# Performance work log

Measured on AMD Instinct MI355X. Metric: run time of the kernel, lower is better.

## Reference

```python
import jax, jax.numpy as jnp
import numpy as np

N = 20000
E = 320000
NODE_DIM = 9
EDGE_DIM = 4
HID = 64
EHID = 32  # hidden_dim // 2, edge feature dim inside GAT layers
HEADS = 4
OUT_DIM = 256
NUM_LAYERS = 3


def layer_norm(x, g, b, eps=1e-5):
    m = jnp.mean(x, axis=-1, keepdims=True)
    v = jnp.mean((x - m) ** 2, axis=-1, keepdims=True)
    return (x - m) / jnp.sqrt(v + eps) * g + b


def setup_inputs():
    key = jax.random.key(0)
    ks = iter(jax.random.split(key, 48))
    def w(shape, scale=0.1):
        return jax.random.normal(next(ks), shape, dtype=jnp.float32) * scale
    inp = {
        "x": jax.random.normal(next(ks), (N, NODE_DIM), dtype=jnp.float32),
        "edge_attr": jax.random.normal(next(ks), (E, EDGE_DIM), dtype=jnp.float32),
        "edge_index": jax.random.randint(next(ks), (2, E), 0, N, dtype=jnp.int32),
        # node encoder: Linear(9,32)+ReLU+Linear(32,64)+LayerNorm(64)
        "ne_w1": w((NODE_DIM, 32)), "ne_b1": jnp.zeros((32,), jnp.float32),
        "ne_w2": w((32, HID)), "ne_b2": jnp.zeros((HID,), jnp.float32),
        "ne_g": jnp.ones((HID,), jnp.float32), "ne_beta": jnp.zeros((HID,), jnp.float32),
        # edge encoder: Linear(4,16)+ReLU+Linear(16,32)+LayerNorm(32)
        "ee_w1": w((EDGE_DIM, 16)), "ee_b1": jnp.zeros((16,), jnp.float32),
        "ee_w2": w((16, EHID)), "ee_b2": jnp.zeros((EHID,), jnp.float32),
        "ee_g": jnp.ones((EHID,), jnp.float32), "ee_beta": jnp.zeros((EHID,), jnp.float32),
        # risk attention: Linear(96,64)+Tanh+Linear(64,1)+Sigmoid
        "ra_w1": w((HID + EHID, HID)), "ra_b1": jnp.zeros((HID,), jnp.float32),
        "ra_w2": w((HID, 1)), "ra_b2": jnp.zeros((1,), jnp.float32),
        # GAT layers (stacked over NUM_LAYERS; identical shapes)
        "gat_wl": w((NUM_LAYERS, HID, HEADS * HID)),       # linear (no bias)
        "gat_wa": w((NUM_LAYERS, 2 * HID + EHID)),          # attention (out=1, no bias)
        "gat_we": w((NUM_LAYERS, EHID, HEADS * HID)),       # edge_transform (no bias)
        "gat_wo": w((NUM_LAYERS, HID, HID)),                # output_transform weight
        "gat_wob": jnp.zeros((NUM_LAYERS, HID), jnp.float32),
        # output layer: Linear(64,128)+ReLU+Linear(128,256)+LayerNorm(256)
        "ow_1": w((HID, 128)), "ob_1": jnp.zeros((128,), jnp.float32),
        "ow_2": w((128, OUT_DIM)), "ob_2": jnp.zeros((OUT_DIM,), jnp.float32),
        "o_g": jnp.ones((OUT_DIM,), jnp.float32), "o_beta": jnp.zeros((OUT_DIM,), jnp.float32),
    }
    return inp


def reference(x, edge_attr, edge_index,
              ne_w1, ne_b1, ne_w2, ne_b2, ne_g, ne_beta,
              ee_w1, ee_b1, ee_w2, ee_b2, ee_g, ee_beta,
              ra_w1, ra_b1, ra_w2, ra_b2,
              gat_wl, gat_wa, gat_we, gat_wo, gat_wob,
              ow_1, ob_1, ow_2, ob_2, o_g, o_beta):
    row, col = edge_index[0], edge_index[1]
    # encoders
    h = layer_norm(jax.nn.relu(x @ ne_w1 + ne_b1) @ ne_w2 + ne_b2, ne_g, ne_beta)            # [N, 64]
    ef = layer_norm(jax.nn.relu(edge_attr @ ee_w1 + ee_b1) @ ee_w2 + ee_b2, ee_g, ee_beta)   # [E, 32]
    # risk weights per edge
    ri = jnp.concatenate([h[row], ef], axis=1)                                                # [E, 96]
    rw = jax.nn.sigmoid(jnp.tanh(ri @ ra_w1 + ra_b1) @ ra_w2 + ra_b2)                         # [E, 1]
    xh = h
    for l in range(NUM_LAYERS):
        xproj = (xh @ gat_wl[l]).reshape(N, HEADS, HID)                                       # [N, H, 64]
        emsg = (ef @ gat_we[l]).reshape(E, HEADS, HID)                                        # [E, H, 64]
        # attention Linear(2*64+32 -> 1) split into three slices; avoids materializing the
        # [E, H, 160] concat. Same math: cat([x_i, x_j, ef]) @ wa.
        wa_i = gat_wa[l][:HID]
        wa_j = gat_wa[l][HID:2 * HID]
        wa_e = gat_wa[l][2 * HID:]
        x_j = xproj[col]                                                                      # [E, H, 64]
        alpha = xproj[row] @ wa_i + x_j @ wa_j + (ef @ wa_e)[:, None]                         # [E, H]
        alpha = jnp.where(alpha >= 0, alpha, 0.2 * alpha)  # leaky_relu(0.2)
        alpha = alpha * rw                                  # risk modulation (broadcast [E,1])
        alpha = jax.nn.softmax(alpha, axis=0)               # softmax over ALL edges per head (as in torch code)
        agg = jax.ops.segment_sum(alpha[:, :, None] * (x_j + emsg), col, num_segments=N)      # [N, H, 64]
        xh = jax.nn.relu(agg.mean(axis=1) @ gat_wo[l] + gat_wob[l])                           # [N, 64]
    out = layer_norm(jax.nn.relu(xh @ ow_1 + ob_1) @ ow_2 + ob_2, o_g, o_beta)                # [N, 256]
    return out
```

## Files before the change

kernel.cpp:

```cpp
#include <hip/hip_runtime.h>
#include <math.h>

#define NN 20000
#define EE 320000
#define HID 64
#define EHID 32
#define HEADS 4

__device__ __forceinline__ float fast_tanh(float x) {
  float e = __expf(2.f * x);
  return 1.f - 2.f * __builtin_amdgcn_rcpf(e + 1.f);
}
__device__ __forceinline__ float fast_sigmoid(float x) {
  return __builtin_amdgcn_rcpf(1.f + __expf(-x));
}
__device__ __forceinline__ float bcast8(float v, int q) {
  switch (q) {
    case 0: return __int_as_float(__builtin_amdgcn_ds_swizzle(__float_as_int(v), (0 << 5) | 0x18));
    case 1: return __int_as_float(__builtin_amdgcn_ds_swizzle(__float_as_int(v), (1 << 5) | 0x18));
    case 2: return __int_as_float(__builtin_amdgcn_ds_swizzle(__float_as_int(v), (2 << 5) | 0x18));
    case 3: return __int_as_float(__builtin_amdgcn_ds_swizzle(__float_as_int(v), (3 << 5) | 0x18));
    case 4: return __int_as_float(__builtin_amdgcn_ds_swizzle(__float_as_int(v), (4 << 5) | 0x18));
    case 5: return __int_as_float(__builtin_amdgcn_ds_swizzle(__float_as_int(v), (5 << 5) | 0x18));
    case 6: return __int_as_float(__builtin_amdgcn_ds_swizzle(__float_as_int(v), (6 << 5) | 0x18));
    default: return __int_as_float(__builtin_amdgcn_ds_swizzle(__float_as_int(v), (7 << 5) | 0x18));
  }
}

__global__ __launch_bounds__(256) void k_node_enc(
    const float* __restrict__ x, const float* __restrict__ w1, const float* __restrict__ b1,
    const float* __restrict__ w2, const float* __restrict__ b2,
    const float* __restrict__ g, const float* __restrict__ beta,
    float* __restrict__ h) {
  int n = blockIdx.x * blockDim.x + threadIdx.x;
  if (n >= NN) return;
  float xin[9];
#pragma unroll
  for (int k = 0; k < 9; k++) xin[k] = x[n * 9 + k];
  float hid[32];
#pragma unroll
  for (int j = 0; j < 32; j++) {
    float a = b1[j];
#pragma unroll
    for (int k = 0; k < 9; k++) a += xin[k] * w1[k * 32 + j];
    hid[j] = fmaxf(a, 0.f);
  }
  float o[64];
  float s = 0.f;
  for (int j = 0; j < 64; j++) {
    float a = b2[j];
#pragma unroll
    for (int k = 0; k < 32; k++) a += hid[k] * w2[k * 64 + j];
    o[j] = a;
    s += a;
  }
  float m = s * (1.f / 64.f);
  float v = 0.f;
  for (int j = 0; j < 64; j++) { float d = o[j] - m; v += d * d; }
  v *= (1.f / 64.f);
  float inv = rsqrtf(v + 1e-5f);
#pragma unroll
  for (int j4 = 0; j4 < 16; j4++) {
    float4 r;
    r.x = (o[j4 * 4 + 0] - m) * inv * g[j4 * 4 + 0] + beta[j4 * 4 + 0];
    r.y = (o[j4 * 4 + 1] - m) * inv * g[j4 * 4 + 1] + beta[j4 * 4 + 1];
    r.z = (o[j4 * 4 + 2] - m) * inv * g[j4 * 4 + 2] + beta[j4 * 4 + 2];
    r.w = (o[j4 * 4 + 3] - m) * inv * g[j4 * 4 + 3] + beta[j4 * 4 + 3];
    ((float4*)&h[n * 64])[j4] = r;
  }
}

__global__ __launch_bounds__(256) void k_hist(const int* __restrict__ ei, int* __restrict__ counts) {
  int e = blockIdx.x * 256 + threadIdx.x;
  if (e < EE) atomicAdd(&counts[ei[EE + e]], 1);
}
__global__ __launch_bounds__(1024) void k_scan(
    const int* __restrict__ counts, int* __restrict__ rowptr, int* __restrict__ cursor) {
  __shared__ int wsum[16];
  int t = threadIdx.x, lane = t & 63, w = t >> 6;
  const int CH = 20;
  int base_i = t * CH;
  int local = 0;
  for (int i = 0; i < CH; i++) {
    int idx = base_i + i;
    if (idx < NN) local += counts[idx];
  }
  int v = local;
#pragma unroll
  for (int off = 1; off < 64; off <<= 1) {
    int u = __shfl_up(v, off);
    if (lane >= off) v += u;
  }
  if (lane == 63) wsum[w] = v;
  __syncthreads();
  int wbase = 0;
  for (int i = 0; i < w; i++) wbase += wsum[i];
  int run = wbase + v - local;
  for (int i = 0; i < CH; i++) {
    int idx = base_i + i;
    if (idx < NN) {
      rowptr[idx] = run;
      cursor[idx] = run;
      run += counts[idx];
    }
  }
  if (t == 1023) rowptr[NN] = EE;
}

__global__ __launch_bounds__(256) void k_edge_enc(
    const float* __restrict__ ea, const float* __restrict__ w1, const float* __restrict__ b1,
    const float* __restrict__ w2, const float* __restrict__ b2,
    const float* __restrict__ g, const float* __restrict__ beta,
    const float* __restrict__ gat_wa, const int* __restrict__ ei,
    int* __restrict__ cursor,
    float* __restrict__ efs, float4* __restrict__ devs4, int2* __restrict__ rcs) {
  int e = blockIdx.x * blockDim.x + threadIdx.x;
  if (e >= EE) return;
  int row = ei[e], col = ei[EE + e];
  int pos = atomicAdd(&cursor[col], 1);
  float4 xin = ((const float4*)ea)[e];
  float hid[16];
#pragma unroll
  for (int j = 0; j < 16; j++) {
    float a = b1[j];
    a += xin.x * w1[0 * 16 + j];
    a += xin.y * w1[1 * 16 + j];
    a += xin.z * w1[2 * 16 + j];
    a += xin.w * w1[3 * 16 + j];
    hid[j] = fmaxf(a, 0.f);
  }
  float o[32];
  float s = 0.f;
#pragma unroll
  for (int j = 0; j < 32; j++) {
    float a = b2[j];
#pragma unroll
    for (int k = 0; k < 16; k++) a += hid[k] * w2[k * 32 + j];
    o[j] = a;
    s += a;
  }
  float m = s * (1.f / 32.f);
  float v = 0.f;
#pragma unroll
  for (int j = 0; j < 32; j++) { float d = o[j] - m; v += d * d; }
  v *= (1.f / 32.f);
  float inv = rsqrtf(v + 1e-5f);
  float d0 = 0.f, d1 = 0.f, d2 = 0.f;
  float vn[32];
#pragma unroll
  for (int j = 0; j < 32; j++) {
    vn[j] = (o[j] - m) * inv * g[j] + beta[j];
    d0 += vn[j] * gat_wa[0 * 160 + 128 + j];
    d1 += vn[j] * gat_wa[1 * 160 + 128 + j];
    d2 += vn[j] * gat_wa[2 * 160 + 128 + j];
  }
#pragma unroll
  for (int j4 = 0; j4 < 8; j4++) {
    float4 r;
    r.x = vn[j4 * 4 + 0]; r.y = vn[j4 * 4 + 1]; r.z = vn[j4 * 4 + 2]; r.w = vn[j4 * 4 + 3];
    ((float4*)&efs[(size_t)pos * 32])[j4] = r;
  }
  devs4[pos] = make_float4(d0, d1, d2, 0.f);
  rcs[pos] = make_int2(row, col);
}

__global__ __launch_bounds__(256) void k_risk_node(
    const float* __restrict__ h, const float* __restrict__ w1, const float* __restrict__ b1,
    float* __restrict__ hnode) {
  __shared__ float xsT[64][20];
  int t = threadIdx.x;
  int n0 = blockIdx.x * 16;
  const float4* h4 = (const float4*)h;
  {
    int m = t & 15, k4 = t >> 4;
    float4 xv = h4[(n0 + m) * 16 + k4];
    xsT[k4 * 4 + 0][m] = xv.x;
    xsT[k4 * 4 + 1][m] = xv.y;
    xsT[k4 * 4 + 2][m] = xv.z;
    xsT[k4 * 4 + 3][m] = xv.w;
  }
  __syncthreads();
  int j = t & 63, grp = t >> 6;
  float bv = b1[j];
  float a0 = bv, a1 = bv, a2 = bv, a3 = bv;
  for (int k = 0; k < 64; k++) {
    float wv = w1[k * 64 + j];
    float4 xv = *(const float4*)&xsT[k][grp * 4];
    a0 += xv.x * wv; a1 += xv.y * wv; a2 += xv.z * wv; a3 += xv.w * wv;
  }
  hnode[(n0 + grp * 4 + 0) * 64 + j] = a0;
  hnode[(n0 + grp * 4 + 1) * 64 + j] = a1;
  hnode[(n0 + grp * 4 + 2) * 64 + j] = a2;
  hnode[(n0 + grp * 4 + 3) * 64 + j] = a3;
}

__global__ __launch_bounds__(256) void k_risk_edge(
    const float* __restrict__ hnode, const float* __restrict__ efs, const int2* __restrict__ rcs,
    const float* __restrict__ w1e, const float* __restrict__ w2, const float* __restrict__ b2_,
    float* __restrict__ rws) {
  int t = threadIdx.x, lane = t & 63;
  int s = lane & 7;
  int p = blockIdx.x * 256 + t;
  int myrow = rcs[p].x;
  const float4* hnode4 = (const float4*)hnode;
  const float4* efs4 = (const float4*)efs;
  const float4* w1e4 = (const float4*)w1e;
  const float4* w24 = (const float4*)w2;
  float ev[32];
#pragma unroll
  for (int i = 0; i < 8; i++) {
    float4 tmp = efs4[(size_t)p * 8 + i];
    ev[i * 4 + 0] = tmp.x; ev[i * 4 + 1] = tmp.y; ev[i * 4 + 2] = tmp.z; ev[i * 4 + 3] = tmp.w;
  }
  int rowq[8];
#pragma unroll
  for (int q = 0; q < 8; q++)
    rowq[q] = __float_as_int(bcast8(__int_as_float(myrow), q));
  float acc[8][8];
#pragma unroll
  for (int q = 0; q < 8; q++) {
    float4 ha = hnode4[(size_t)rowq[q] * 16 + s * 2];
    float4 hb = hnode4[(size_t)rowq[q] * 16 + s * 2 + 1];
    acc[q][0] = ha.x; acc[q][1] = ha.y; acc[q][2] = ha.z; acc[q][3] = ha.w;
    acc[q][4] = hb.x; acc[q][5] = hb.y; acc[q][6] = hb.z; acc[q][7] = hb.w;
  }
#pragma unroll
  for (int k = 0; k < 32; k++) {
    float4 wa4 = w1e4[k * 16 + s * 2];
    float4 wb4 = w1e4[k * 16 + s * 2 + 1];
#pragma unroll
    for (int q = 0; q < 8; q++) {
      float ekq = bcast8(ev[k], q);
      acc[q][0] += ekq * wa4.x; acc[q][1] += ekq * wa4.y;
      acc[q][2] += ekq * wa4.z; acc[q][3] += ekq * wa4.w;
      acc[q][4] += ekq * wb4.x; acc[q][5] += ekq * wb4.y;
      acc[q][6] += ekq * wb4.z; acc[q][7] += ekq * wb4.w;
    }
  }
  float4 wva = w24[s * 2], wvb = w24[s * 2 + 1];
  float tq[8];
#pragma unroll
  for (int q = 0; q < 8; q++) {
    tq[q] = fast_tanh(acc[q][0]) * wva.x + fast_tanh(acc[q][1]) * wva.y +
            fast_tanh(acc[q][2]) * wva.z + fast_tanh(acc[q][3]) * wva.w +
            fast_tanh(acc[q][4]) * wvb.x + fast_tanh(acc[q][5]) * wvb.y +
            fast_tanh(acc[q][6]) * wvb.z + fast_tanh(acc[q][7]) * wvb.w;
  }
#pragma unroll
  for (int q = 0; q < 8; q++) {
    tq[q] += __shfl_xor(tq[q], 1);
    tq[q] += __shfl_xor(tq[q], 2);
    tq[q] += __shfl_xor(tq[q], 4);
  }
  float mine = tq[0];
  mine = (s == 1) ? tq[1] : mine;
  mine = (s == 2) ? tq[2] : mine;
  mine = (s == 3) ? tq[3] : mine;
  mine = (s == 4) ? tq[4] : mine;
  mine = (s == 5) ? tq[5] : mine;
  mine = (s == 6) ? tq[6] : mine;
  mine = (s == 7) ? tq[7] : mine;
  rws[p] = fast_sigmoid(mine + b2_[0]);
}

__global__ __launch_bounds__(256) void k_xproj(
    const float* __restrict__ xh, const float* __restrict__ wl, const float* __restrict__ wa,
    float* __restrict__ xproj, float* __restrict__ di, float* __restrict__ dj) {
  __shared__ float xsT[64][20];
  int t = threadIdx.x, lane = t & 63, w = t >> 6;
  int n0 = blockIdx.x * 16;
  const float4* xh4 = (const float4*)xh;
  {
    int m = t & 15, k4 = t >> 4;
    float4 xv = xh4[(n0 + m) * 16 + k4];
    xsT[k4 * 4 + 0][m] = xv.x;
    xsT[k4 * 4 + 1][m] = xv.y;
    xsT[k4 * 4 + 2][m] = xv.z;
    xsT[k4 * 4 + 3][m] = xv.w;
  }
  __syncthreads();
  const float4* wl4 = (const float4*)wl;
  float4 acc0 = {0,0,0,0}, acc1 = {0,0,0,0}, acc2 = {0,0,0,0}, acc3 = {0,0,0,0};
  for (int k = 0; k < 64; k++) {
    float4 xv = *(const float4*)&xsT[k][4 * w];
    float4 wv = wl4[k * 64 + lane];
    acc0.x += xv.x * wv.x; acc0.y += xv.x * wv.y; acc0.z += xv.x * wv.z; acc0.w += xv.x * wv.w;
    acc1.x += xv.y * wv.x; acc1.y += xv.y * wv.y; acc1.z += xv.y * wv.z; acc1.w += xv.y * wv.w;
    acc2.x += xv.z * wv.x; acc2.y += xv.z * wv.y; acc2.z += xv.z * wv.z; acc2.w += xv.z * wv.w;
    acc3.x += xv.w * wv.x; acc3.y += xv.w * wv.y; acc3.z += xv.w * wv.z; acc3.w += xv.w * wv.w;
  }
  float4* xp4 = (float4*)xproj;
  xp4[(size_t)(n0 + 4 * w + 0) * 64 + lane] = acc0;
  xp4[(size_t)(n0 + 4 * w + 1) * 64 + lane] = acc1;
  xp4[(size_t)(n0 + 4 * w + 2) * 64 + lane] = acc2;
  xp4[(size_t)(n0 + 4 * w + 3) * 64 + lane] = acc3;
  float4 wi4 = ((const float4*)wa)[lane];
  float4 wj4 = ((const float4*)wa)[16 + lane];
  float4 accq[4] = {acc0, acc1, acc2, acc3};
#pragma unroll
  for (int q = 0; q < 4; q++) {
    float vi = accq[q].x * wi4.x + accq[q].y * wi4.y + accq[q].z * wi4.z + accq[q].w * wi4.w;
    float vj = accq[q].x * wj4.x + accq[q].y * wj4.y + accq[q].z * wj4.z + accq[q].w * wj4.w;
#pragma unroll
    for (int off = 1; off < 16; off <<= 1) { vi += __shfl_xor(vi, off); vj += __shfl_xor(vj, off); }
    if ((lane & 15) == 0) {
      di[(n0 + 4 * w + q) * 4 + (lane >> 4)] = vi;
      dj[(n0 + 4 * w + q) * 4 + (lane >> 4)] = vj;
    }
  }
}

__global__ __launch_bounds__(256) void k_pexp(
    const int2* __restrict__ rcs, const float4* __restrict__ devs4,
    const float* __restrict__ rws, const float* __restrict__ di,
    const float* __restrict__ dj, int layer,
    float4* __restrict__ ps4, float* __restrict__ gsum_l) {
  __shared__ float wred[4][4];
  int t = threadIdx.x, lane = t & 63, w = t >> 6;
  int i = blockIdx.x * 256 + t;
  int2 rc = rcs[i];
  float4 dv = devs4[i];
  float dev = (layer == 0) ? dv.x : ((layer == 1) ? dv.y : dv.z);
  float rv = rws[i];
  float4 dr = ((const float4*)di)[rc.x];
  float4 djc = ((const float4*)dj)[rc.y];
  float z0 = dr.x + djc.x + dev, z1 = dr.y + djc.y + dev;
  float z2 = dr.z + djc.z + dev, z3 = dr.w + djc.w + dev;
  z0 = ((z0 >= 0.f) ? z0 : 0.2f * z0) * rv;
  z1 = ((z1 >= 0.f) ? z1 : 0.2f * z1) * rv;
  z2 = ((z2 >= 0.f) ? z2 : 0.2f * z2) * rv;
  z3 = ((z3 >= 0.f) ? z3 : 0.2f * z3) * rv;
  float4 pv;
  pv.x = __expf(z0); pv.y = __expf(z1); pv.z = __expf(z2); pv.w = __expf(z3);
  ps4[i] = pv;
  float sh[4] = {pv.x, pv.y, pv.z, pv.w};
#pragma unroll
  for (int h = 0; h < 4; h++) {
    float v = sh[h];
#pragma unroll
    for (int off = 32; off; off >>= 1) v += __shfl_xor(v, off);
    if (lane == 0) wred[w][h] = v;
  }
  __syncthreads();
  if (t < 4) atomicAdd(&gsum_l[t], wred[0][t] + wred[1][t] + wred[2][t] + wred[3][t]);
}

template <bool DO_XPROJ>
__global__ __launch_bounds__(256) void k_aggupdate(
    const int* __restrict__ rowptr, const float4* __restrict__ ps4,
    const float* __restrict__ efs, const float* __restrict__ gsum_l,
    const float* __restrict__ xproj,
    const float* __restrict__ we, const float* __restrict__ wo, const float* __restrict__ wob,
    const float* __restrict__ wl_next, const float* __restrict__ wa_next,
    float* __restrict__ xh_out, float* __restrict__ xproj_out,
    float* __restrict__ di, float* __restrict__ dj) {
  __shared__ float tsT[128][20];
  __shared__ float usT[64][20];
  __shared__ float xhT[64][20];
  __shared__ float ss[16][4];
  int t = threadIdx.x, lane = t & 63, wv = t >> 6;
  int n0 = blockIdx.x * 16;
  float4 gs = *((const float4*)gsum_l);
  float inv0 = 1.0f / gs.x, inv1 = 1.0f / gs.y, inv2 = 1.0f / gs.z, inv3 = 1.0f / gs.w;
  int c = lane & 31, slot = lane >> 5;
#pragma unroll
  for (int q = 0; q < 4; q++) {
    int n = n0 + wv * 4 + q;
    int beg = rowptr[n], end = rowptr[n + 1];
    float a0 = 0.f, a1 = 0.f, a2 = 0.f, a3 = 0.f;
    float s0 = 0.f, s1 = 0.f, s2 = 0.f, s3 = 0.f;
    int i = beg + slot;
    for (; i + 2 < end; i += 4) {
      float4 pa = ps4[i];
      float eva = efs[(size_t)i * 32 + c];
      float4 pb = ps4[i + 2];
      float evb = efs[(size_t)(i + 2) * 32 + c];
      a0 += pa.x * eva + pb.x * evb;
      a1 += pa.y * eva + pb.y * evb;
      a2 += pa.z * eva + pb.z * evb;
      a3 += pa.w * eva + pb.w * evb;
      s0 += pa.x + pb.x; s1 += pa.y + pb.y;
      s2 += pa.z + pb.z; s3 += pa.w + pb.w;
    }
    if (i < end) {
      float4 pa = ps4[i];
      float eva = efs[(size_t)i * 32 + c];
      a0 += pa.x * eva; a1 += pa.y * eva; a2 += pa.z * eva; a3 += pa.w * eva;
      s0 += pa.x; s1 += pa.y; s2 += pa.z; s3 += pa.w;
    }
    a0 += __shfl_xor(a0, 32); a1 += __shfl_xor(a1, 32);
    a2 += __shfl_xor(a2, 32); a3 += __shfl_xor(a3, 32);
    s0 += __shfl_xor(s0, 32); s1 += __shfl_xor(s1, 32);
    s2 += __shfl_xor(s2, 32); s3 += __shfl_xor(s3, 32);
    if (slot == 0) {
      int m = wv * 4 + q;
      tsT[0 * 32 + c][m] = a0 * inv0;
      tsT[1 * 32 + c][m] = a1 * inv1;
      tsT[2 * 32 + c][m] = a2 * inv2;
      tsT[3 * 32 + c][m] = a3 * inv3;
      if (c < 4) {
        float sv = (c == 0) ? s0 : (c == 1) ? s1 : (c == 2) ? s2 : s3;
        float iv = (c == 0) ? inv0 : (c == 1) ? inv1 : (c == 2) ? inv2 : inv3;
        ss[m][c] = sv * iv;
      }
    }
  }
  __syncthreads();
  int j = lane, grp = wv;
  float u0 = 0.f, u1 = 0.f, u2 = 0.f, u3 = 0.f;
#pragma unroll
  for (int h = 0; h < 4; h++) {
    u0 += xproj[(n0 + grp * 4 + 0) * 256 + h * 64 + j] * ss[grp * 4 + 0][h];
    u1 += xproj[(n0 + grp * 4 + 1) * 256 + h * 64 + j] * ss[grp * 4 + 1][h];
    u2 += xproj[(n0 + grp * 4 + 2) * 256 + h * 64 + j] * ss[grp * 4 + 2][h];
    u3 += xproj[(n0 + grp * 4 + 3) * 256 + h * 64 + j] * ss[grp * 4 + 3][h];
  }
  for (int hc = 0; hc < 128; hc++) {
    float wv2 = we[(hc & 31) * 256 + (hc >> 5) * 64 + j];
    float4 tv = *(const float4*)&tsT[hc][grp * 4];
    u0 += tv.x * wv2; u1 += tv.y * wv2; u2 += tv.z * wv2; u3 += tv.w * wv2;
  }
  *(float4*)&usT[j][grp * 4] = make_float4(u0 * 0.25f, u1 * 0.25f, u2 * 0.25f, u3 * 0.25f);
  __syncthreads();
  float ob = wob[j];
  float o0 = ob, o1 = ob, o2 = ob, o3 = ob;
  for (int k = 0; k < 64; k++) {
    float wv2 = wo[k * 64 + j];
    float4 uv = *(const float4*)&usT[k][grp * 4];
    o0 += uv.x * wv2; o1 += uv.y * wv2; o2 += uv.z * wv2; o3 += uv.w * wv2;
  }
  o0 = fmaxf(o0, 0.f); o1 = fmaxf(o1, 0.f); o2 = fmaxf(o2, 0.f); o3 = fmaxf(o3, 0.f);
  if (!DO_XPROJ) {
    xh_out[(n0 + grp * 4 + 0) * 64 + j] = o0;
    xh_out[(n0 + grp * 4 + 1) * 64 + j] = o1;
    xh_out[(n0 + grp * 4 + 2) * 64 + j] = o2;
    xh_out[(n0 + grp * 4 + 3) * 64 + j] = o3;
    return;
  }
  xhT[j][grp * 4 + 0] = o0;
  xhT[j][grp * 4 + 1] = o1;
  xhT[j][grp * 4 + 2] = o2;
  xhT[j][grp * 4 + 3] = o3;
  __syncthreads();
  const float4* wl4 = (const float4*)wl_next;
  float4 acc0 = {0,0,0,0}, acc1 = {0,0,0,0}, acc2 = {0,0,0,0}, acc3 = {0,0,0,0};
  for (int k = 0; k < 64; k++) {
    float4 xv = *(const float4*)&xhT[k][4 * wv];
    float4 wv2 = wl4[k * 64 + lane];
    acc0.x += xv.x * wv2.x; acc0.y += xv.x * wv2.y; acc0.z += xv.x * wv2.z; acc0.w += xv.x * wv2.w;
    acc1.x += xv.y * wv2.x; acc1.y += xv.y * wv2.y; acc1.z += xv.y * wv2.z; acc1.w += xv.y * wv2.w;
    acc2.x += xv.z * wv2.x; acc2.y += xv.z * wv2.y; acc2.z += xv.z * wv2.z; acc2.w += xv.z * wv2.w;
    acc3.x += xv.w * wv2.x; acc3.y += xv.w * wv2.y; acc3.z += xv.w * wv2.z; acc3.w += xv.w * wv2.w;
  }
  float4* xp4 = (float4*)xproj_out;
  xp4[(size_t)(n0 + 4 * wv + 0) * 64 + lane] = acc0;
  xp4[(size_t)(n0 + 4 * wv + 1) * 64 + lane] = acc1;
  xp4[(size_t)(n0 + 4 * wv + 2) * 64 + lane] = acc2;
  xp4[(size_t)(n0 + 4 * wv + 3) * 64 + lane] = acc3;
  float4 wi4 = ((const float4*)wa_next)[lane];
  float4 wj4 = ((const float4*)wa_next)[16 + lane];
  float4 accq[4] = {acc0, acc1, acc2, acc3};
#pragma unroll
  for (int q = 0; q < 4; q++) {
    float vi = accq[q].x * wi4.x + accq[q].y * wi4.y + accq[q].z * wi4.z + accq[q].w * wi4.w;
    float vj = accq[q].x * wj4.x + accq[q].y * wj4.y + accq[q].z * wj4.z + accq[q].w * wj4.w;
#pragma unroll
    for (int off = 1; off < 16; off <<= 1) { vi += __shfl_xor(vi, off); vj += __shfl_xor(vj, off); }
    if ((lane & 15) == 0) {
      di[(n0 + 4 * wv + q) * 4 + (lane >> 4)] = vi;
      dj[(n0 + 4 * wv + q) * 4 + (lane >> 4)] = vj;
    }
  }
}

#define OPN 16
__global__ __launch_bounds__(256) void k_out(
    const float* __restrict__ xh, const float* __restrict__ w1, const float* __restrict__ b1,
    const float* __restrict__ w2, const float* __restrict__ b2,
    const float* __restrict__ g, const float* __restrict__ beta,
    float* __restrict__ out) {
  __shared__ float xsT[64][20];
  __shared__ float hsT[128][20];
  int t = threadIdx.x, lane = t & 63, w = t >> 6;
  int n0 = blockIdx.x * OPN;
  const float4* xh4 = (const float4*)xh;
  {
    int m = t & 15, k4 = t >> 4;
    float4 xv = xh4[(n0 + m) * 16 + k4];
    xsT[k4 * 4 + 0][m] = xv.x;
    xsT[k4 * 4 + 1][m] = xv.y;
    xsT[k4 * 4 + 2][m] = xv.z;
    xsT[k4 * 4 + 3][m] = xv.w;
  }
  __syncthreads();
  {
    float b0 = b1[lane], b64 = b1[64 + lane];
    float4 h0 = make_float4(b0, b0, b0, b0);
    float4 h1 = make_float4(b64, b64, b64, b64);
    for (int k = 0; k < 64; k++) {
      float4 xv = *(const float4*)&xsT[k][4 * w];
      float wa = w1[k * 128 + lane];
      float wb = w1[k * 128 + 64 + lane];
      h0.x += xv.x * wa; h0.y += xv.y * wa; h0.z += xv.z * wa; h0.w += xv.w * wa;
      h1.x += xv.x * wb; h1.y += xv.y * wb; h1.z += xv.z * wb; h1.w += xv.w * wb;
    }
    h0.x = fmaxf(h0.x, 0.f); h0.y = fmaxf(h0.y, 0.f); h0.z = fmaxf(h0.z, 0.f); h0.w = fmaxf(h0.w, 0.f);
    h1.x = fmaxf(h1.x, 0.f); h1.y = fmaxf(h1.y, 0.f); h1.z = fmaxf(h1.z, 0.f); h1.w = fmaxf(h1.w, 0.f);
    *(float4*)&hsT[lane][4 * w] = h0;
    *(float4*)&hsT[64 + lane][4 * w] = h1;
  }
  __syncthreads();
  const float4* w24 = (const float4*)w2;
  float4 b2v = ((const float4*)b2)[lane];
  float4 o0 = b2v, o1 = b2v, o2 = b2v, o3 = b2v;
  for (int k = 0; k < 128; k++) {
    float4 hv = *(const float4*)&hsT[k][4 * w];
    float4 wv = w24[k * 64 + lane];
    o0.x += hv.x * wv.x; o0.y += hv.x * wv.y; o0.z += hv.x * wv.z; o0.w += hv.x * wv.w;
    o1.x += hv.y * wv.x; o1.y += hv.y * wv.y; o1.z += hv.y * wv.z; o1.w += hv.y * wv.w;
    o2.x += hv.z * wv.x; o2.y += hv.z * wv.y; o2.z += hv.z * wv.z; o2.w += hv.z * wv.w;
    o3.x += hv.w * wv.x; o3.y += hv.w * wv.y; o3.z += hv.w * wv.z; o3.w += hv.w * wv.w;
  }
  float4 gv = ((const float4*)g)[lane];
  float4 bv = ((const float4*)beta)[lane];
  float4* out4 = (float4*)out;
  float4 oq[4] = {o0, o1, o2, o3};
#pragma unroll
  for (int q = 0; q < 4; q++) {
    float s1 = oq[q].x + oq[q].y + oq[q].z + oq[q].w;
    float s2 = oq[q].x * oq[q].x + oq[q].y * oq[q].y + oq[q].z * oq[q].z + oq[q].w * oq[q].w;
#pragma unroll
    for (int off = 1; off < 64; off <<= 1) { s1 += __shfl_xor(s1, off); s2 += __shfl_xor(s2, off); }
    float mean = s1 * (1.f / 256.f);
    float var = s2 * (1.f / 256.f) - mean * mean;
    float inv = rsqrtf(var + 1e-5f);
    float4 r;
    r.x = (oq[q].x - mean) * inv * gv.x + bv.x;
    r.y = (oq[q].y - mean) * inv * gv.y + bv.y;
    r.z = (oq[q].z - mean) * inv * gv.z + bv.z;
    r.w = (oq[q].w - mean) * inv * gv.w + bv.w;
    out4[(size_t)(n0 + 4 * w + q) * 64 + lane] = r;
  }
}

extern "C" void kernel_launch(void* const* d_in, const int* in_sizes, int n_in,
                              void* d_out, int out_size, void* d_ws, size_t ws_size,
                              hipStream_t stream) {
  const float* x         = (const float*)d_in[0];
  const float* edge_attr = (const float*)d_in[1];
  const int*   ei        = (const int*)d_in[2];
  const float* ne_w1 = (const float*)d_in[3];
  const float* ne_b1 = (const float*)d_in[4];
  const float* ne_w2 = (const float*)d_in[5];
  const float* ne_b2 = (const float*)d_in[6];
  const float* ne_g  = (const float*)d_in[7];
  const float* ne_be = (const float*)d_in[8];
  const float* ee_w1 = (const float*)d_in[9];
  const float* ee_b1 = (const float*)d_in[10];
  const float* ee_w2 = (const float*)d_in[11];
  const float* ee_b2 = (const float*)d_in[12];
  const float* ee_g  = (const float*)d_in[13];
  const float* ee_be = (const float*)d_in[14];
  const float* ra_w1 = (const float*)d_in[15];
  const float* ra_b1 = (const float*)d_in[16];
  const float* ra_w2 = (const float*)d_in[17];
  const float* ra_b2 = (const float*)d_in[18];
  const float* gat_wl  = (const float*)d_in[19];
  const float* gat_wa  = (const float*)d_in[20];
  const float* gat_we  = (const float*)d_in[21];
  const float* gat_wo  = (const float*)d_in[22];
  const float* gat_wob = (const float*)d_in[23];
  const float* ow_1 = (const float*)d_in[24];
  const float* ob_1 = (const float*)d_in[25];
  const float* ow_2 = (const float*)d_in[26];
  const float* ob_2 = (const float*)d_in[27];
  const float* o_g  = (const float*)d_in[28];
  const float* o_be = (const float*)d_in[29];
  float* out = (float*)d_out;

  char* wsb = (char*)d_ws;
  size_t off = 0;
  auto af = [&](size_t elems) -> float* { float* p = (float*)(wsb + off); off += elems * sizeof(float); return p; };
  auto ai = [&](size_t elems) -> int*   { int*   p = (int*)(wsb + off);   off += elems * sizeof(int);   return p; };

  float* h      = af((size_t)NN * 64);
  float* xh2    = af((size_t)NN * 64);
  float* efs    = af((size_t)EE * 32);
  float* devs   = af((size_t)EE * 4);
  float* rws    = af((size_t)EE);
  float* ps     = af((size_t)EE * 4);
  float* xprojA = af((size_t)NN * 256);
  float* xprojB = af((size_t)NN * 256);
  float* di     = af((size_t)NN * 4);
  float* dj     = af((size_t)NN * 4);
  float* gsum   = af(12);
  int* rcs    = ai(2 * (size_t)EE);
  int* counts = ai(NN);
  int* rowptr = ai(NN + 1);
  int* cursor = ai(NN);
  float* hnode = xprojB;
  (void)ws_size; (void)n_in; (void)in_sizes; (void)out_size;

  hipMemsetAsync(counts, 0, NN * sizeof(int), stream);
  hipMemsetAsync(gsum, 0, 12 * sizeof(float), stream);
  k_hist<<<EE / 256, 256, 0, stream>>>(ei, counts);
  k_node_enc<<<(NN + 255) / 256, 256, 0, stream>>>(x, ne_w1, ne_b1, ne_w2, ne_b2, ne_g, ne_be, h);
  k_scan<<<1, 1024, 0, stream>>>(counts, rowptr, cursor);
  k_edge_enc<<<EE / 256, 256, 0, stream>>>(edge_attr, ee_w1, ee_b1, ee_w2, ee_b2, ee_g, ee_be,
                                           gat_wa, ei, cursor, efs, (float4*)devs, (int2*)rcs);
  k_risk_node<<<NN / 16, 256, 0, stream>>>(h, ra_w1, ra_b1, hnode);
  k_risk_edge<<<EE / 256, 256, 0, stream>>>(hnode, efs, (const int2*)rcs,
                                            ra_w1 + 64 * 64, ra_w2, ra_b2, rws);
  k_xproj<<<NN / 16, 256, 0, stream>>>(h, gat_wl, gat_wa, xprojA, di, dj);

  float* xp_cur = xprojA;
  float* xp_nxt = xprojB;
  for (int l = 0; l < 3; l++) {
    const float* we  = gat_we + (size_t)l * 32 * 256;
    const float* wo  = gat_wo + (size_t)l * 64 * 64;
    const float* wob = gat_wob + (size_t)l * 64;
    float* gsum_l = gsum + l * 4;

    k_pexp<<<EE / 256, 256, 0, stream>>>((const int2*)rcs, (const float4*)devs, rws,
                                         di, dj, l, (float4*)ps, gsum_l);
    if (l < 2) {
      const float* wl_n = gat_wl + (size_t)(l + 1) * 64 * 256;
      const float* wa_n = gat_wa + (size_t)(l + 1) * 160;
      k_aggupdate<true><<<NN / 16, 256, 0, stream>>>(
          rowptr, (const float4*)ps, efs, gsum_l, xp_cur, we, wo, wob, wl_n, wa_n,
          nullptr, xp_nxt, di, dj);
      float* tmp = xp_cur; xp_cur = xp_nxt; xp_nxt = tmp;
    } else {
      k_aggupdate<false><<<NN / 16, 256, 0, stream>>>(
          rowptr, (const float4*)ps, efs, gsum_l, xp_cur, we, wo, wob, nullptr, nullptr,
          xh2, nullptr, nullptr, nullptr);
    }
  }

  k_out<<<NN / OPN, 256, 0, stream>>>(xh2, ow_1, ob_1, ow_2, ob_2, o_g, o_be, out);
}
```

Baseline: 486.6 us.

## Replace shared-memory transposes with wave readlane broadcasts in node GEMM kernels

The small per-node matmuls in risk_node, xproj, aggupdate and the output layer no longer stage activations transposed in LDS behind __syncthreads. Each wave now keeps its four rows in registers and broadcasts element k to all lanes with readlane while looping over k. This removes LDS traffic, block barriers and shared-memory use, which may raise occupancy. The cost is a scalar readlane per row per k step, which needs a uniform k and fully unrolled loops, so scalar-unit throughput could become the limit.

```diff
diff --git a/kernel.cpp b/kernel.cpp
--- a/kernel.cpp
+++ b/kernel.cpp
@@ -13,6 +13,9 @@
 }
 __device__ __forceinline__ float fast_sigmoid(float x) {
   return __builtin_amdgcn_rcpf(1.f + __expf(-x));
+}
+__device__ __forceinline__ float rlane(float v, int l) {
+  return __int_as_float(__builtin_amdgcn_readlane(__float_as_int(v), l));
 }
 __device__ __forceinline__ float bcast8(float v, int q) {
   switch (q) {
@@ -167,31 +170,20 @@
 __global__ __launch_bounds__(256) void k_risk_node(
     const float* __restrict__ h, const float* __restrict__ w1, const float* __restrict__ b1,
     float* __restrict__ hnode) {
-  __shared__ float xsT[64][20];
-  int t = threadIdx.x;
+  int t = threadIdx.x, lane = t & 63, w = t >> 6;
   int n0 = blockIdx.x * 16;
-  const float4* h4 = (const float4*)h;
-  {
-    int m = t & 15, k4 = t >> 4;
-    float4 xv = h4[(n0 + m) * 16 + k4];
-    xsT[k4 * 4 + 0][m] = xv.x;
-    xsT[k4 * 4 + 1][m] = xv.y;
-    xsT[k4 * 4 + 2][m] = xv.z;
-    xsT[k4 * 4 + 3][m] = xv.w;
-  }
-  __syncthreads();
-  int j = t & 63, grp = t >> 6;
-  float bv = b1[j];
-  float a0 = bv, a1 = bv, a2 = bv, a3 = bv;
+  float xq[4];
+#pragma unroll
+  for (int q = 0; q < 4; q++) xq[q] = h[(size_t)(n0 + 4 * w + q) * 64 + lane];
+  float bv = b1[lane];
+  float a[4] = {bv, bv, bv, bv};
   for (int k = 0; k < 64; k++) {
-    float wv = w1[k * 64 + j];
-    float4 xv = *(const float4*)&xsT[k][grp * 4];
-    a0 += xv.x * wv; a1 += xv.y * wv; a2 += xv.z * wv; a3 += xv.w * wv;
-  }
-  hnode[(n0 + grp * 4 + 0) * 64 + j] = a0;
-  hnode[(n0 + grp * 4 + 1) * 64 + j] = a1;
-  hnode[(n0 + grp * 4 + 2) * 64 + j] = a2;
-  hnode[(n0 + grp * 4 + 3) * 64 + j] = a3;
+    float wv = w1[k * 64 + lane];
+#pragma unroll
+    for (int q = 0; q < 4; q++) a[q] += rlane(xq[q], k) * wv;
+  }
+#pragma unroll
+  for (int q = 0; q < 4; q++) hnode[(size_t)(n0 + 4 * w + q) * 64 + lane] = a[q];
 }
 
 __global__ __launch_bounds__(256) void k_risk_edge(
@@ -266,41 +258,32 @@
 __global__ __launch_bounds__(256) void k_xproj(
     const float* __restrict__ xh, const float* __restrict__ wl, const float* __restrict__ wa,
     float* __restrict__ xproj, float* __restrict__ di, float* __restrict__ dj) {
-  __shared__ float xsT[64][20];
   int t = threadIdx.x, lane = t & 63, w = t >> 6;
   int n0 = blockIdx.x * 16;
-  const float4* xh4 = (const float4*)xh;
-  {
-    int m = t & 15, k4 = t >> 4;
-    float4 xv = xh4[(n0 + m) * 16 + k4];
-    xsT[k4 * 4 + 0][m] = xv.x;
-    xsT[k4 * 4 + 1][m] = xv.y;
-    xsT[k4 * 4 + 2][m] = xv.z;
-    xsT[k4 * 4 + 3][m] = xv.w;
-  }
-  __syncthreads();
+  float xq[4];
+#pragma unroll
+  for (int q = 0; q < 4; q++) xq[q] = xh[(size_t)(n0 + 4 * w + q) * 64 + lane];
   const float4* wl4 = (const float4*)wl;
-  float4 acc0 = {0,0,0,0}, acc1 = {0,0,0,0}, acc2 = {0,0,0,0}, acc3 = {0,0,0,0};
+  float4 xp[4];
+#pragma unroll
+  for (int q = 0; q < 4; q++) xp[q] = make_float4(0.f, 0.f, 0.f, 0.f);
   for (int k = 0; k < 64; k++) {
-    float4 xv = *(const float4*)&xsT[k][4 * w];
     float4 wv = wl4[k * 64 + lane];
-    acc0.x += xv.x * wv.x; acc0.y += xv.x * wv.y; acc0.z += xv.x * wv.z; acc0.w += xv.x * wv.w;
-    acc1.x += xv.y * wv.x; acc1.y += xv.y * wv.y; acc1.z += xv.y * wv.z; acc1.w += xv.y * wv.w;
-    acc2.x += xv.z * wv.x; acc2.y += xv.z * wv.y; acc2.z += xv.z * wv.z; acc2.w += xv.z * wv.w;
-    acc3.x += xv.w * wv.x; acc3.y += xv.w * wv.y; acc3.z += xv.w * wv.z; acc3.w += xv.w * wv.w;
+#pragma unroll
+    for (int q = 0; q < 4; q++) {
+      float s = rlane(xq[q], k);
+      xp[q].x += s * wv.x; xp[q].y += s * wv.y; xp[q].z += s * wv.z; xp[q].w += s * wv.w;
+    }
   }
   float4* xp4 = (float4*)xproj;
-  xp4[(size_t)(n0 + 4 * w + 0) * 64 + lane] = acc0;
-  xp4[(size_t)(n0 + 4 * w + 1) * 64 + lane] = acc1;
-  xp4[(size_t)(n0 + 4 * w + 2) * 64 + lane] = acc2;
-  xp4[(size_t)(n0 + 4 * w + 3) * 64 + lane] = acc3;
+#pragma unroll
+  for (int q = 0; q < 4; q++) xp4[(size_t)(n0 + 4 * w + q) * 64 + lane] = xp[q];
   float4 wi4 = ((const float4*)wa)[lane];
   float4 wj4 = ((const float4*)wa)[16 + lane];
-  float4 accq[4] = {acc0, acc1, acc2, acc3};
 #pragma unroll
   for (int q = 0; q < 4; q++) {
-    float vi = accq[q].x * wi4.x + accq[q].y * wi4.y + accq[q].z * wi4.z + accq[q].w * wi4.w;
-    float vj = accq[q].x * wj4.x + accq[q].y * wj4.y + accq[q].z * wj4.z + accq[q].w * wj4.w;
+    float vi = xp[q].x * wi4.x + xp[q].y * wi4.y + xp[q].z * wi4.z + xp[q].w * wi4.w;
+    float vj = xp[q].x * wj4.x + xp[q].y * wj4.y + xp[q].z * wj4.z + xp[q].w * wj4.w;
 #pragma unroll
     for (int off = 1; off < 16; off <<= 1) { vi += __shfl_xor(vi, off); vj += __shfl_xor(vj, off); }
     if ((lane & 15) == 0) {
@@ -354,15 +337,13 @@
     const float* __restrict__ wl_next, const float* __restrict__ wa_next,
     float* __restrict__ xh_out, float* __restrict__ xproj_out,
     float* __restrict__ di, float* __restrict__ dj) {
-  __shared__ float tsT[128][20];
-  __shared__ float usT[64][20];
-  __shared__ float xhT[64][20];
-  __shared__ float ss[16][4];
   int t = threadIdx.x, lane = t & 63, wv = t >> 6;
   int n0 = blockIdx.x * 16;
   float4 gs = *((const float4*)gsum_l);
   float inv0 = 1.0f / gs.x, inv1 = 1.0f / gs.y, inv2 = 1.0f / gs.z, inv3 = 1.0f / gs.w;
   int c = lane & 31, slot = lane >> 5;
+  float ta[4][4];
+  float sa[4][4];
 #pragma unroll
   for (int q = 0; q < 4; q++) {
     int n = n0 + wv * 4 + q;
@@ -392,78 +373,63 @@
     a2 += __shfl_xor(a2, 32); a3 += __shfl_xor(a3, 32);
     s0 += __shfl_xor(s0, 32); s1 += __shfl_xor(s1, 32);
     s2 += __shfl_xor(s2, 32); s3 += __shfl_xor(s3, 32);
-    if (slot == 0) {
-      int m = wv * 4 + q;
-      tsT[0 * 32 + c][m] = a0 * inv0;
-      tsT[1 * 32 + c][m] = a1 * inv1;
-      tsT[2 * 32 + c][m] = a2 * inv2;
-      tsT[3 * 32 + c][m] = a3 * inv3;
-      if (c < 4) {
-        float sv = (c == 0) ? s0 : (c == 1) ? s1 : (c == 2) ? s2 : s3;
-        float iv = (c == 0) ? inv0 : (c == 1) ? inv1 : (c == 2) ? inv2 : inv3;
-        ss[m][c] = sv * iv;
-      }
-    }
-  }
-  __syncthreads();
-  int j = lane, grp = wv;
-  float u0 = 0.f, u1 = 0.f, u2 = 0.f, u3 = 0.f;
-#pragma unroll
-  for (int h = 0; h < 4; h++) {
-    u0 += xproj[(n0 + grp * 4 + 0) * 256 + h * 64 + j] * ss[grp * 4 + 0][h];
-    u1 += xproj[(n0 + grp * 4 + 1) * 256 + h * 64 + j] * ss[grp * 4 + 1][h];
-    u2 += xproj[(n0 + grp * 4 + 2) * 256 + h * 64 + j] * ss[grp * 4 + 2][h];
-    u3 += xproj[(n0 + grp * 4 + 3) * 256 + h * 64 + j] * ss[grp * 4 + 3][h];
-  }
-  for (int hc = 0; hc < 128; hc++) {
-    float wv2 = we[(hc & 31) * 256 + (hc >> 5) * 64 + j];
-    float4 tv = *(const float4*)&tsT[hc][grp * 4];
-    u0 += tv.x * wv2; u1 += tv.y * wv2; u2 += tv.z * wv2; u3 += tv.w * wv2;
-  }
-  *(float4*)&usT[j][grp * 4] = make_float4(u0 * 0.25f, u1 * 0.25f, u2 * 0.25f, u3 * 0.25f);
-  __syncthreads();
-  float ob = wob[j];
-  float o0 = ob, o1 = ob, o2 = ob, o3 = ob;
+    ta[q][0] = a0 * inv0; ta[q][1] = a1 * inv1; ta[q][2] = a2 * inv2; ta[q][3] = a3 * inv3;
+    sa[q][0] = s0 * inv0; sa[q][1] = s1 * inv1; sa[q][2] = s2 * inv2; sa[q][3] = s3 * inv3;
+  }
+  float u[4];
+#pragma unroll
+  for (int q = 0; q < 4; q++) {
+    size_t base = (size_t)(n0 + wv * 4 + q) * 256;
+    u[q] = xproj[base + 0 * 64 + lane] * sa[q][0]
+         + xproj[base + 1 * 64 + lane] * sa[q][1]
+         + xproj[base + 2 * 64 + lane] * sa[q][2]
+         + xproj[base + 3 * 64 + lane] * sa[q][3];
+  }
+  for (int cc = 0; cc < 32; cc++) {
+#pragma unroll
+    for (int h = 0; h < 4; h++) {
+      float wvv = we[cc * 256 + h * 64 + lane];
+#pragma unroll
+      for (int q = 0; q < 4; q++) u[q] += rlane(ta[q][h], cc) * wvv;
+    }
+  }
+#pragma unroll
+  for (int q = 0; q < 4; q++) u[q] *= 0.25f;
+  float ob = wob[lane];
+  float o[4] = {ob, ob, ob, ob};
   for (int k = 0; k < 64; k++) {
-    float wv2 = wo[k * 64 + j];
-    float4 uv = *(const float4*)&usT[k][grp * 4];
-    o0 += uv.x * wv2; o1 += uv.y * wv2; o2 += uv.z * wv2; o3 += uv.w * wv2;
-  }
-  o0 = fmaxf(o0, 0.f); o1 = fmaxf(o1, 0.f); o2 = fmaxf(o2, 0.f); o3 = fmaxf(o3, 0.f);
+    float wvv = wo[k * 64 + lane];
+#pragma unroll
+    for (int q = 0; q < 4; q++) o[q] += rlane(u[q], k) * wvv;
+  }
+#pragma unroll
+  for (int q = 0; q < 4; q++) o[q] = fmaxf(o[q], 0.f);
   if (!DO_XPROJ) {
-    xh_out[(n0 + grp * 4 + 0) * 64 + j] = o0;
-    xh_out[(n0 + grp * 4 + 1) * 64 + j] = o1;
-    xh_out[(n0 + grp * 4 + 2) * 64 + j] = o2;
-    xh_out[(n0 + grp * 4 + 3) * 64 + j] = o3;
+#pragma unroll
+    for (int q = 0; q < 4; q++) xh_out[(size_t)(n0 + wv * 4 + q) * 64 + lane] = o[q];
     return;
   }
-  xhT[j][grp * 4 + 0] = o0;
-  xhT[j][grp * 4 + 1] = o1;
-  xhT[j][grp * 4 + 2] = o2;
-  xhT[j][grp * 4 + 3] = o3;
-  __syncthreads();
   const float4* wl4 = (const float4*)wl_next;
-  float4 acc0 = {0,0,0,0}, acc1 = {0,0,0,0}, acc2 = {0,0,0,0}, acc3 = {0,0,0,0};
+  float4 xp[4];
+#pragma unroll
+  for (int q = 0; q < 4; q++) xp[q] = make_float4(0.f, 0.f, 0.f, 0.f);
   for (int k = 0; k < 64; k++) {
-    float4 xv = *(const float4*)&xhT[k][4 * wv];
-    float4 wv2 = wl4[k * 64 + lane];
-    acc0.x += xv.x * wv2.x; acc0.y += xv.x * wv2.y; acc0.z += xv.x * wv2.z; acc0.w += xv.x * wv2.w;
-    acc1.x += xv.y * wv2.x; acc1.y += xv.y * wv2.y; acc1.z += xv.y * wv2.z; acc1.w += xv.y * wv2.w;
-    acc2.x += xv.z * wv2.x; acc2.y += xv.z * wv2.y; acc2.z += xv.z * wv2.z; acc2.w += xv.z * wv2.w;
-    acc3.x += xv.w * wv2.x; acc3.y += xv.w * wv2.y; acc3.z += xv.w * wv2.z; acc3.w += xv.w * wv2.w;
+    float4 wvv = wl4[k * 64 + lane];
+#pragma unroll
+    for (int q = 0; q < 4; q++) {
+      float s = rlane(o[q], k);
+      xp[q].x += s * wvv.x; xp[q].y += s * wvv.y; xp[q].z += s * wvv.z; xp[q].w += s * wvv.w;
+    }
   }
   float4* xp4 = (float4*)xproj_out;
-  xp4[(size_t)(n0 + 4 * wv + 0) * 64 + lane] = acc0;
-  xp4[(size_t)(n0 + 4 * wv + 1) * 64 + lane] = acc1;
-  xp4[(size_t)(n0 + 4 * wv + 2) * 64 + lane] = acc2;
-  xp4[(size_t)(n0 + 4 * wv + 3) * 64 + lane] = acc3;
+#pragma unroll
+  for (int q = 0; q < 4; q++) xp4[(size_t)(n0 + 4 * wv + q) * 64 + lane] = xp[q];
   float4 wi4 = ((const float4*)wa_next)[lane];
   float4 wj4 = ((const float4*)wa_next)[16 + lane];
-  float4 accq[4] = {acc0, acc1, acc2, acc3};
 #pragma unroll
   for (int q = 0; q < 4; q++) {
-    float vi = accq[q].x * wi4.x + accq[q].y * wi4.y + accq[q].z * wi4.z + accq[q].w * wi4.w;
-    float vj = accq[q].x * wj4.x + accq[q].y * wj4.y + accq[q].z * wj4.z + accq[q].w * wj4.w;
+    float vi = xp[q].x * wi4.x + xp[q].y * wi4.y + xp[q].z * wi4.z + xp[q].w * wi4.w;
+    float vj = xp[q].x * wj4.x + xp[q].y * wj4.y + xp[q].z * wj4.z + xp[q].w * wj4.w;
 #pragma unroll
     for (int off = 1; off < 16; off <<= 1) { vi += __shfl_xor(vi, off); vj += __shfl_xor(vj, off); }
     if ((lane & 15) == 0) {
@@ -479,66 +445,62 @@
     const float* __restrict__ w2, const float* __restrict__ b2,
     const float* __restrict__ g, const float* __restrict__ beta,
     float* __restrict__ out) {
-  __shared__ float xsT[64][20];
-  __shared__ float hsT[128][20];
   int t = threadIdx.x, lane = t & 63, w = t >> 6;
   int n0 = blockIdx.x * OPN;
-  const float4* xh4 = (const float4*)xh;
-  {
-    int m = t & 15, k4 = t >> 4;
-    float4 xv = xh4[(n0 + m) * 16 + k4];
-    xsT[k4 * 4 + 0][m] = xv.x;
-    xsT[k4 * 4 + 1][m] = xv.y;
-    xsT[k4 * 4 + 2][m] = xv.z;
-    xsT[k4 * 4 + 3][m] = xv.w;
-  }
-  __syncthreads();
-  {
-    float b0 = b1[lane], b64 = b1[64 + lane];
-    float4 h0 = make_float4(b0, b0, b0, b0);
-    float4 h1 = make_float4(b64, b64, b64, b64);
-    for (int k = 0; k < 64; k++) {
-      float4 xv = *(const float4*)&xsT[k][4 * w];
-      float wa = w1[k * 128 + lane];
-      float wb = w1[k * 128 + 64 + lane];
-      h0.x += xv.x * wa; h0.y += xv.y * wa; h0.z += xv.z * wa; h0.w += xv.w * wa;
-      h1.x += xv.x * wb; h1.y += xv.y * wb; h1.z += xv.z * wb; h1.w += xv.w * wb;
-    }
-    h0.x = fmaxf(h0.x, 0.f); h0.y = fmaxf(h0.y, 0.f); h0.z = fmaxf(h0.z, 0.f); h0.w = fmaxf(h0.w, 0.f);
-    h1.x = fmaxf(h1.x, 0.f); h1.y = fmaxf(h1.y, 0.f); h1.z = fmaxf(h1.z, 0.f); h1.w = fmaxf(h1.w, 0.f);
-    *(float4*)&hsT[lane][4 * w] = h0;
-    *(float4*)&hsT[64 + lane][4 * w] = h1;
-  }
-  __syncthreads();
+  float xq[4];
+#pragma unroll
+  for (int q = 0; q < 4; q++) xq[q] = xh[(size_t)(n0 + 4 * w + q) * 64 + lane];
+  float b0 = b1[lane], b64 = b1[64 + lane];
+  float h0[4] = {b0, b0, b0, b0};
+  float h1[4] = {b64, b64, b64, b64};
+  for (int k = 0; k < 64; k++) {
+    float wa = w1[k * 128 + lane];
+    float wb = w1[k * 128 + 64 + lane];
+#pragma unroll
+    for (int q = 0; q < 4; q++) {
+      float s = rlane(xq[q], k);
+      h0[q] += s * wa;
+      h1[q] += s * wb;
+    }
+  }
+#pragma unroll
+  for (int q = 0; q < 4; q++) { h0[q] = fmaxf(h0[q], 0.f); h1[q] = fmaxf(h1[q], 0.f); }
   const float4* w24 = (const float4*)w2;
   float4 b2v = ((const float4*)b2)[lane];
-  float4 o0 = b2v, o1 = b2v, o2 = b2v, o3 = b2v;
-  for (int k = 0; k < 128; k++) {
-    float4 hv = *(const float4*)&hsT[k][4 * w];
-    float4 wv = w24[k * 64 + lane];
-    o0.x += hv.x * wv.x; o0.y += hv.x * wv.y; o0.z += hv.x * wv.z; o0.w += hv.x * wv.w;
-    o1.x += hv.y * wv.x; o1.y += hv.y * wv.y; o1.z += hv.y * wv.z; o1.w += hv.y * wv.w;
-    o2.x += hv.z * wv.x; o2.y += hv.z * wv.y; o2.z += hv.z * wv.z; o2.w += hv.z * wv.w;
-    o3.x += hv.w * wv.x; o3.y += hv.w * wv.y; o3.z += hv.w * wv.z; o3.w += hv.w * wv.w;
+  float4 o[4] = {b2v, b2v, b2v, b2v};
+  for (int k = 0; k < 64; k++) {
+    float4 wvv = w24[k * 64 + lane];
+#pragma unroll
+    for (int q = 0; q < 4; q++) {
+      float s = rlane(h0[q], k);
+      o[q].x += s * wvv.x; o[q].y += s * wvv.y; o[q].z += s * wvv.z; o[q].w += s * wvv.w;
+    }
+  }
+  for (int k = 0; k < 64; k++) {
+    float4 wvv = w24[(64 + k) * 64 + lane];
+#pragma unroll
+    for (int q = 0; q < 4; q++) {
+      float s = rlane(h1[q], k);
+      o[q].x += s * wvv.x; o[q].y += s * wvv.y; o[q].z += s * wvv.z; o[q].w += s * wvv.w;
+    }
   }
   float4 gv = ((const float4*)g)[lane];
   float4 bv = ((const float4*)beta)[lane];
   float4* out4 = (float4*)out;
-  float4 oq[4] = {o0, o1, o2, o3};
 #pragma unroll
   for (int q = 0; q < 4; q++) {
-    float s1 = oq[q].x + oq[q].y + oq[q].z + oq[q].w;
-    float s2 = oq[q].x * oq[q].x + oq[q].y * oq[q].y + oq[q].z * oq[q].z + oq[q].w * oq[q].w;
+    float s1 = o[q].x + o[q].y + o[q].z + o[q].w;
+    float s2 = o[q].x * o[q].x + o[q].y * o[q].y + o[q].z * o[q].z + o[q].w * o[q].w;
 #pragma unroll
     for (int off = 1; off < 64; off <<= 1) { s1 += __shfl_xor(s1, off); s2 += __shfl_xor(s2, off); }
     float mean = s1 * (1.f / 256.f);
     float var = s2 * (1.f / 256.f) - mean * mean;
     float inv = rsqrtf(var + 1e-5f);
     float4 r;
-    r.x = (oq[q].x - mean) * inv * gv.x + bv.x;
-    r.y = (oq[q].y - mean) * inv * gv.y + bv.y;
-    r.z = (oq[q].z - mean) * inv * gv.z + bv.z;
-    r.w = (oq[q].w - mean) * inv * gv.w + bv.w;
+    r.x = (o[q].x - mean) * inv * gv.x + bv.x;
+    r.y = (o[q].y - mean) * inv * gv.y + bv.y;
+    r.z = (o[q].z - mean) * inv * gv.z + bv.z;
+    r.w = (o[q].w - mean) * inv * gv.w + bv.w;
     out4[(size_t)(n0 + 4 * w + q) * 64 + lane] = r;
   }
 }
```

Measured after the change: 513.1 us. 1.05x slower.
